# Performance work log

Hardware: AMD Instinct MI355X
Metric: run time of the kernel (lower is better)

The kernel has to match this reference:

```python
import jax, jax.numpy as jnp
import numpy as np

G, N, H = 64, 512, 64          # graphs, nodes/graph, hidden
NT = G * N                     # total nodes
DEG = 32
ET = NT * DEG                  # total edges
KP = int(np.ceil(0.7 * N))     # TopKPooling keep per graph (359)
NP2 = G * KP                   # nodes after pooling
F_IN, NC, NA = 128, 2, 6
seg = jax.ops.segment_sum


def graph_norm(h, batch, num_g, w, b, ms, eps=1e-5):
    cnt = seg(jnp.ones((h.shape[0], 1), h.dtype), batch, num_segments=num_g)
    mean = seg(h, batch, num_segments=num_g) / cnt
    hc = h - ms * mean[batch]
    var = seg(hc * hc, batch, num_segments=num_g) / cnt
    return w * hc / jnp.sqrt(var[batch] + eps) + b


def sage(h, src, tgt, valid, Ws, Wn, b, n_nodes):
    # PyG SAGEConv (mean aggr): out_i = x_i@Ws + mean_{j->i} x_j @ Wn + b
    msg = h[src] * valid[:, None]
    agg = seg(msg, tgt, num_segments=n_nodes)
    deg = seg(valid, tgt, num_segments=n_nodes)
    return h @ Ws + (agg / jnp.maximum(deg, 1.0)[:, None]) @ Wn + b


def setup_inputs() -> dict:
    key = jax.random.key(0)
    ks = jax.random.split(key, 20)
    offs = (jnp.arange(G) * N)[:, None]
    src = (jax.random.randint(ks[0], (G, N * DEG), 0, N) + offs).reshape(-1)
    tgt = (jax.random.randint(ks[1], (G, N * DEG), 0, N) + offs).reshape(-1)
    edge_index = jnp.stack([src, tgt])  # within-graph edges

    def lin(k, fi, fo):
        return jax.random.normal(k, (fi, fo), jnp.float32) / np.sqrt(fi)

    return {
        "x": jax.random.normal(ks[2], (NT, F_IN), jnp.float32),
        "edge_index": edge_index,
        "edge_attr": jax.random.uniform(ks[3], (ET,), jnp.float32),
        "coords": jax.random.normal(ks[4], (NT, 3), jnp.float32),
        "anatomical_class": jax.random.randint(ks[5], (NT,), 0, NA),
        "Bk_table": jax.random.normal(ks[6], (NA, H * H), jnp.float32) * 0.05,
        "pos_W": lin(ks[7], 3, H), "pos_b": jnp.zeros((H,), jnp.float32),
        "W1_self": lin(ks[8], F_IN, H), "W1_neigh": lin(ks[9], F_IN, H),
        "b1": jnp.zeros((H,), jnp.float32),
        "gn1_w": jnp.ones((H,), jnp.float32), "gn1_b": jnp.zeros((H,), jnp.float32),
        "gn1_ms": jnp.ones((H,), jnp.float32),
        "pool_p": jax.random.normal(ks[10], (H,), jnp.float32),
        "W2_self": lin(ks[11], H, H), "W2_neigh": lin(ks[12], H, H),
        "b2": jnp.zeros((H,), jnp.float32),
        "gn2_w": jnp.ones((H,), jnp.float32), "gn2_b": jnp.zeros((H,), jnp.float32),
        "gn2_ms": jnp.ones((H,), jnp.float32),
        "lin1_W": lin(ks[13], 3 * H, H), "lin1_b": jnp.zeros((H,), jnp.float32),
        "lin2_W": lin(ks[14], H, NC), "lin2_b": jnp.zeros((NC,), jnp.float32),
    }


def reference(x, edge_index, edge_attr, coords, anatomical_class, Bk_table,
              pos_W, pos_b, W1_self, W1_neigh, b1, gn1_w, gn1_b, gn1_ms,
              pool_p, W2_self, W2_neigh, b2, gn2_w, gn2_b, gn2_ms,
              lin1_W, lin1_b, lin2_W, lin2_b):
    row, col = edge_index[0], edge_index[1]
    batch = jnp.repeat(jnp.arange(G), N)
    # ---- stage 1: anatomical propagation kernel ----
    e = coords @ pos_W + pos_b                                 # [NT, H]
    Ae = seg(edge_attr[:, None] * e[col], row, num_segments=NT)  # SpMM adj @ e
    Bk = Bk_table[anatomical_class].reshape(NT, H, H)
    delta = jnp.einsum('nd,nhd->nh', Ae, Bk)                   # bmm(Ae, Bk^T)
    ones_e = jnp.ones((ET,), x.dtype)
    h = sage(x, row, col, ones_e, W1_self, W1_neigh, b1, NT)
    h = jax.nn.elu(graph_norm(h, batch, G, gn1_w, gn1_b, gn1_ms))
    h = h + delta
    h = jnp.einsum('nij,nj->ni', Bk + delta[:, :, None], h)    # propagate_message
    # ---- TopK pooling (equal-sized graphs) ----
    score = (h @ pool_p) / jnp.linalg.norm(pool_p)
    vals, idx = jax.lax.top_k(score.reshape(G, N), KP)
    perm = (idx + (jnp.arange(G) * N)[:, None]).reshape(-1)    # [NP2]
    h = h[perm] * jnp.tanh(vals).reshape(-1)[:, None]
    batch2 = jnp.repeat(jnp.arange(G), KP)
    node_map = jnp.full((NT,), -1, jnp.int32).at[perm].set(jnp.arange(NP2, dtype=jnp.int32))
    s2, t2 = node_map[row], node_map[col]
    valid = ((s2 >= 0) & (t2 >= 0)).astype(h.dtype)            # masked edge filter
    s2 = jnp.where(s2 >= 0, s2, 0)
    t2 = jnp.where(t2 >= 0, t2, 0)
    # ---- stage 2 ----
    e2 = coords[perm] @ pos_W + pos_b
    Bk2 = Bk_table[anatomical_class[perm]].reshape(NP2, H, H)
    Ae2 = seg(valid[:, None] * e2[t2], s2, num_segments=NP2)   # edge_attr = ones
    delta2 = jnp.einsum('nd,nhd->nh', Ae2, Bk2)
    h = h + delta2
    h = jnp.einsum('nij,nj->ni', Bk2 + delta2[:, :, None], h)
    h = sage(h, s2, t2, valid, W2_self, W2_neigh, b2, NP2)
    h = jax.nn.elu(graph_norm(h, batch2, G, gn2_w, gn2_b, gn2_ms))
    # ---- readout ----
    cnt = seg(jnp.ones((NP2, 1), h.dtype), batch2, num_segments=G)
    hsum = seg(h, batch2, num_segments=G)
    g = jnp.concatenate([hsum / cnt,
                         jax.ops.segment_max(h, batch2, num_segments=G),
                         hsum], axis=1)
    g = jax.nn.relu(g @ lin1_W + lin1_b)
    return jax.nn.log_softmax(g @ lin2_W + lin2_b, axis=1)
```

## Files before the change

### kernel.cpp

```cpp
#include <hip/hip_runtime.h>
#include <math.h>

#define G_    64
#define N_    512
#define H_    64
#define NT_   32768
#define ET_   1048576
#define EPG_  16384
#define KP_   359
#define NP2_  22976
#define FIN_  128
#define ESL_  2048
#define BPB_  (EPG_/ESL_)

__global__ __launch_bounds__(256)
void k_histprep(const int* __restrict__ row, const int* __restrict__ col,
                int* __restrict__ histR8, int* __restrict__ histC8,
                const float* __restrict__ Bk, const float* __restrict__ posW,
                const float* __restrict__ posb,
                float* __restrict__ BkT, float* __restrict__ PT) {
    int b = blockIdx.x, t = threadIdx.x;
    if (b < G_ * BPB_) {
        __shared__ int hr[N_], hc[N_];
        int g = b >> 3, s = b & (BPB_ - 1);
        for (int i = t; i < N_; i += 256) { hr[i] = 0; hc[i] = 0; }
        __syncthreads();
        int ebase = g * EPG_ + s * ESL_;
        for (int i = t; i < ESL_; i += 256) {
            atomicAdd(&hr[row[ebase + i] & (N_ - 1)], 1);
            atomicAdd(&hc[col[ebase + i] & (N_ - 1)], 1);
        }
        __syncthreads();
        int sbase = (g * BPB_ + s) * N_;
        for (int i = t; i < N_; i += 256) {
            histR8[sbase + i] = hr[i];
            histC8[sbase + i] = hc[i];
        }
    } else if (b < G_ * BPB_ + 96) {
        int idx = (b - G_ * BPB_) * 256 + t;
        int c = idx >> 12, r = idx & 4095;
        int h = r >> 6, d = r & 63;
        BkT[c * 4096 + d * 64 + h] = Bk[c * 4096 + h * 64 + d];
    } else {
        int c = b - (G_ * BPB_ + 96);
        int i = t >> 6, h = t & 63;
        const float* B = Bk + c * 4096 + h * 64;
        float acc = 0.f;
        for (int d = 0; d < 64; d++) {
            float vd = (i < 3) ? posW[i*64 + d] : posb[d];
            acc += B[d] * vd;
        }
        PT[c*256 + i*64 + h] = acc;
    }
}

__global__ __launch_bounds__(256)
void k_scan(const int* __restrict__ histR8, const int* __restrict__ histC8,
            int* __restrict__ rowptr, int* __restrict__ colptr,
            float* __restrict__ deg, int* __restrict__ nmap) {
    __shared__ int hr[N_], hc[N_];
    int g = blockIdx.x, t = threadIdx.x;
    int nbase = g * N_;
    for (int i = t; i < N_; i += 256) {
        int sr = 0, sc = 0;
        #pragma unroll
        for (int s = 0; s < BPB_; s++) {
            sr += histR8[(g * BPB_ + s) * N_ + i];
            sc += histC8[(g * BPB_ + s) * N_ + i];
        }
        hr[i] = sr; hc[i] = sc;
        deg[nbase + i] = (float)sc;
        nmap[nbase + i] = -1;
    }
    __syncthreads();
    int wave = t >> 6, lane = t & 63;
    if (wave < 2) {
        int* h = wave ? hc : hr;
        int base8 = lane * 8;
        int loc[8];
        int tot = 0;
        #pragma unroll
        for (int i = 0; i < 8; i++) { int v = h[base8 + i]; loc[i] = tot; tot += v; }
        int pref = tot;
        for (int off = 1; off < 64; off <<= 1) {
            int u = __shfl_up(pref, off);
            if (lane >= off) pref += u;
        }
        pref -= tot;
        #pragma unroll
        for (int i = 0; i < 8; i++) h[base8 + i] = pref + loc[i];
    }
    __syncthreads();
    int ebase = g * EPG_;
    for (int i = t; i < N_; i += 256) {
        rowptr[nbase + i] = ebase + hr[i];
        colptr[nbase + i] = ebase + hc[i];
    }
    if (g == 0 && t == 0) { rowptr[NT_] = ET_; colptr[NT_] = ET_; }
}

__global__ __launch_bounds__(1024)
void k_scat(const int* __restrict__ row, const int* __restrict__ col,
            const float* __restrict__ ea,
            const int* __restrict__ rowptr, const int* __restrict__ colptr,
            int2* __restrict__ rowcsr, int* __restrict__ colcsr) {
    __shared__ int curR[128], curC[128];
    int g = blockIdx.x >> 2, q = blockIdx.x & 3;
    int t = threadIdx.x;
    int lo = q * 128;
    int nbase = g * N_ + lo;
    if (t < 128) { curR[t] = rowptr[nbase + t]; curC[t] = colptr[nbase + t]; }
    __syncthreads();
    int ebase = g * EPG_;
    for (int i = t; i < EPG_; i += 1024) {
        int rg = row[ebase + i];
        int cg = col[ebase + i];
        int rl = (rg & (N_ - 1)) - lo;
        if ((unsigned)rl < 128u) {
            int pr = atomicAdd(&curR[rl], 1);
            rowcsr[pr] = make_int2(cg, __float_as_int(ea[ebase + i]));
        }
        int cl = (cg & (N_ - 1)) - lo;
        if ((unsigned)cl < 128u) {
            int pc = atomicAdd(&curC[cl], 1);
            colcsr[pc] = rg;
        }
    }
}

__global__ __launch_bounds__(256)
void k_gemm_dual(const float* __restrict__ in, int K,
                 const float* __restrict__ Wa, const float* __restrict__ Wb,
                 const float* __restrict__ bias,
                 float* __restrict__ outA, float* __restrict__ outB) {
    __shared__ float inT[32 * FIN_];
    int row0 = blockIdx.x * 32;
    int t = threadIdx.x;
    for (int idx = t; idx < 32 * K; idx += 256) inT[idx] = in[row0 * K + idx];
    __syncthreads();
    int c = t & 63, rb = t >> 6;
    const float* ip = inT + (rb * 8) * K;
    float aA[8] = {0,0,0,0,0,0,0,0};
    float aB[8] = {0,0,0,0,0,0,0,0};
    for (int k = 0; k < K; k += 4) {
        float wa0 = Wa[(k+0)*64 + c], wa1 = Wa[(k+1)*64 + c];
        float wa2 = Wa[(k+2)*64 + c], wa3 = Wa[(k+3)*64 + c];
        float wb0 = Wb[(k+0)*64 + c], wb1 = Wb[(k+1)*64 + c];
        float wb2 = Wb[(k+2)*64 + c], wb3 = Wb[(k+3)*64 + c];
        #pragma unroll
        for (int r = 0; r < 8; r++) {
            float4 xv = *(const float4*)&ip[r*K + k];
            aA[r] += xv.x*wa0; aB[r] += xv.x*wb0;
            aA[r] += xv.y*wa1; aB[r] += xv.y*wb1;
            aA[r] += xv.z*wa2; aB[r] += xv.z*wb2;
            aA[r] += xv.w*wa3; aB[r] += xv.w*wb3;
        }
    }
    float bv = bias[c];
    #pragma unroll
    for (int r = 0; r < 8; r++) {
        int node = row0 + rb*8 + r;
        outA[node*64 + c] = aA[r];
        outB[node*64 + c] = aB[r] + bv;
    }
}

__global__ __launch_bounds__(256)
void k_edge1f(const int* __restrict__ rowptr, const int2* __restrict__ rcsr,
              const int* __restrict__ colptr, const int* __restrict__ ccsr,
              const float* __restrict__ coords, const float* __restrict__ y,
              float4* __restrict__ nsum, float* __restrict__ agg) {
    int node = blockIdx.x * 4 + (threadIdx.x >> 6);
    int lane = threadIdx.x & 63;
    int rs = rowptr[node], re = rowptr[node + 1];
    float sx = 0.f, sy = 0.f, sz = 0.f, sw = 0.f;
    for (int k = rs + lane; k < re; k += 64) {
        int2 ent = rcsr[k];
        int c = ent.x;
        float w = __int_as_float(ent.y);
        sx += w * coords[c*3+0];
        sy += w * coords[c*3+1];
        sz += w * coords[c*3+2];
        sw += w;
    }
    #pragma unroll
    for (int off = 32; off; off >>= 1) {
        sx += __shfl_xor(sx, off); sy += __shfl_xor(sy, off);
        sz += __shfl_xor(sz, off); sw += __shfl_xor(sw, off);
    }
    if (lane == 0) nsum[node] = make_float4(sx, sy, sz, sw);
    int cs = colptr[node], ce = colptr[node + 1];
    float acc = 0.f;
    #pragma unroll 8
    for (int k = cs; k < ce; k++) {
        int r = ccsr[k];
        acc += y[r*64 + lane];
    }
    agg[node*64 + lane] = acc;
}

__global__ __launch_bounds__(256)
void k_gnstat(const float* __restrict__ hs, const float* __restrict__ agg,
              const float* __restrict__ deg, float* __restrict__ partial,
              int NPG, int CH, int npc) {
    __shared__ float r1[256], r2[256];
    int b = blockIdx.x;
    int g = b / CH, chunk = b % CH;
    int t = threadIdx.x, c = t & 63, grp = t >> 6;
    int n0 = chunk * npc;
    int nend = min(n0 + npc, NPG);
    float s1 = 0.f, s2 = 0.f;
    for (int n = n0 + grp; n < nend; n += 4) {
        int node = g * NPG + n;
        float v = hs[node*64 + c] + agg[node*64 + c] / fmaxf(deg[node], 1.f);
        s1 += v; s2 += v * v;
    }
    r1[t] = s1; r2[t] = s2;
    __syncthreads();
    if (grp == 0) {
        partial[b*128 + c]      = r1[c] + r1[64+c] + r1[128+c] + r1[192+c];
        partial[b*128 + 64 + c] = r2[c] + r2[64+c] + r2[128+c] + r2[192+c];
    }
}

__global__ __launch_bounds__(256)
void k_gnprop(const float* __restrict__ hself, const float* __restrict__ agg,
              const float* __restrict__ deg, const float* __restrict__ partial,
              const float* __restrict__ ms,
              const float* __restrict__ w, const float* __restrict__ b,
              const float4* __restrict__ nsum, const int* __restrict__ cls,
              const float* __restrict__ PT, const float* __restrict__ BkT,
              float* __restrict__ out) {
    __shared__ float hT[256];
    int t = threadIdx.x;
    int node = blockIdx.x * 4 + (t >> 6);
    int lane = t & 63;
    int g = (blockIdx.x * 4) >> 9;
    float s1 = 0.f, s2 = 0.f;
    #pragma unroll
    for (int i = 0; i < 8; i++) {
        s1 += partial[(g*8 + i)*128 + lane];
        s2 += partial[(g*8 + i)*128 + 64 + lane];
    }
    float m  = s1 / (float)N_, q = s2 / (float)N_, msv = ms[lane];
    float var = q - msv * m * m * (2.f - msv);
    float mval = msv * m;
    float istd = rsqrtf(var + 1e-5f);
    float4 s4 = nsum[node];
    int c = cls[node];
    const float* P = PT + c * 256;
    float d = s4.x*P[lane] + s4.y*P[64+lane] + s4.z*P[128+lane] + s4.w*P[192+lane];
    float v = hself[node*64 + lane] + agg[node*64 + lane] / fmaxf(deg[node], 1.f);
    v = w[lane] * (v - mval) * istd + b[lane];
    v = v > 0.f ? v : expm1f(v);
    v += d;
    hT[t] = v;
    __syncthreads();
    float ssum = v;
    #pragma unroll
    for (int off = 32; off; off >>= 1) ssum += __shfl_xor(ssum, off);
    const float* B  = BkT + c * 4096;
    const float* hv = hT + (t & ~63);
    float acc = 0.f;
    #pragma unroll 8
    for (int j = 0; j < 64; j++) acc += B[j*64 + lane] * hv[j];
    out[node*64 + lane] = acc + d * ssum;
}

__global__ __launch_bounds__(512)
void k_topk(const float* __restrict__ hp, const float* __restrict__ p,
            const int* __restrict__ cls, const int* __restrict__ ccsr,
            int* __restrict__ perm, float* __restrict__ tanhv,
            int* __restrict__ node_map, int* __restrict__ class2,
            int* __restrict__ ccsr2) {
    __shared__ float key[N_];
    __shared__ int   idxS[N_];
    __shared__ int   lmap[N_];
    __shared__ float pS[64];
    __shared__ float nrm;
    int g = blockIdx.x, t = threadIdx.x;
    lmap[t] = -1;
    if (t < 64) pS[t] = p[t];
    __syncthreads();
    if (t == 0) {
        float s = 0.f;
        for (int i = 0; i < 64; i++) s += pS[i] * pS[i];
        nrm = sqrtf(s);
    }
    __syncthreads();
    {
        float acc = 0.f;
        const float* hv = hp + (size_t)(g*N_ + t) * 64;
        for (int cdx = 0; cdx < 64; cdx++) acc += hv[cdx] * pS[cdx];
        key[t]  = acc / nrm;
        idxS[t] = t;
    }
    __syncthreads();
    for (int k = 2; k <= N_; k <<= 1) {
        for (int j = k >> 1; j > 0; j >>= 1) {
            int i = t, ixj = i ^ j;
            if (ixj > i) {
                float ki = key[i], kj = key[ixj];
                int   ii = idxS[i], ij = idxS[ixj];
                bool before = (ki > kj) || (ki == kj && ii < ij);
                bool dir = ((i & k) == 0);
                if (dir ? !before : before) {
                    key[i] = kj; key[ixj] = ki;
                    idxS[i] = ij; idxS[ixj] = ii;
                }
            }
            __syncthreads();
        }
    }
    if (t < KP_) {
        int orig  = idxS[t];
        int gnode = g * N_ + orig;
        int pj    = g * KP_ + t;
        perm[pj]     = gnode;
        tanhv[pj]    = tanhf(key[t]);
        node_map[gnode] = pj;
        class2[pj]   = cls[gnode];
        lmap[orig]   = pj;
    }
    __syncthreads();
    int ebase = g * EPG_;
    for (int k = t; k < EPG_; k += 512) {
        int mm = lmap[ccsr[ebase + k] & (N_ - 1)];
        ccsr2[ebase + k] = (mm >= 0) ? mm : NP2_;
    }
}

__global__ __launch_bounds__(256)
void k_s2prop(const int* __restrict__ rowptr, const int2* __restrict__ rcsr,
              const int* __restrict__ colptr, const int* __restrict__ ccsr,
              const int* __restrict__ perm, const int* __restrict__ nmap,
              const float* __restrict__ coords,
              const float* __restrict__ hp, const float* __restrict__ tanhv,
              const int* __restrict__ cls2,
              const float* __restrict__ PT, const float* __restrict__ BkT,
              float* __restrict__ out, float* __restrict__ deg2,
              float* __restrict__ y2zero) {
    __shared__ float hT[256];
    int t = threadIdx.x;
    int j = blockIdx.x * 4 + (t >> 6);
    int lane = t & 63;
    if (blockIdx.x == 0 && t < 64) y2zero[t] = 0.f;
    int orig = perm[j];
    int rs = rowptr[orig], re = rowptr[orig + 1];
    float sx = 0.f, sy = 0.f, sz = 0.f, sw = 0.f;
    for (int k = rs + lane; k < re; k += 64) {
        int c = rcsr[k].x;
        if (nmap[c] >= 0) {
            sx += coords[c*3+0]; sy += coords[c*3+1]; sz += coords[c*3+2];
            sw += 1.f;
        }
    }
    int cs = colptr[orig], ce = colptr[orig + 1];
    float dg = 0.f;
    for (int k = cs + lane; k < ce; k += 64) {
        if (nmap[ccsr[k]] >= 0) dg += 1.f;
    }
    #pragma unroll
    for (int off = 32; off; off >>= 1) {
        sx += __shfl_xor(sx, off); sy += __shfl_xor(sy, off);
        sz += __shfl_xor(sz, off); sw += __shfl_xor(sw, off);
        dg += __shfl_xor(dg, off);
    }
    if (lane == 0) deg2[j] = dg;
    int c = cls2[j];
    const float* P = PT + c * 256;
    float d = sx*P[lane] + sy*P[64+lane] + sz*P[128+lane] + sw*P[192+lane];
    float v = hp[orig*64 + lane] * tanhv[j] + d;
    hT[t] = v;
    __syncthreads();
    float ssum = v;
    #pragma unroll
    for (int off = 32; off; off >>= 1) ssum += __shfl_xor(ssum, off);
    const float* B  = BkT + c * 4096;
    const float* hv = hT + (t & ~63);
    float acc = 0.f;
    #pragma unroll 8
    for (int jj = 0; jj < 64; jj++) acc += B[jj*64 + lane] * hv[jj];
    out[j*64 + lane] = acc + d * ssum;
}

__global__ __launch_bounds__(256)
void k_gagg2(const int* __restrict__ colptr, const int* __restrict__ ccsr2,
             const int* __restrict__ perm, const float* __restrict__ y2,
             float* __restrict__ agg2) {
    int j = blockIdx.x * 4 + (threadIdx.x >> 6);
    int lane = threadIdx.x & 63;
    int orig = perm[j];
    int start = colptr[orig], end = colptr[orig + 1];
    float acc = 0.f;
    #pragma unroll 8
    for (int k = start; k < end; k++) {
        int r = ccsr2[k];
        acc += y2[r*64 + lane];
    }
    agg2[j*64 + lane] = acc;
}

__global__ __launch_bounds__(256)
void k_gnrd(const float* __restrict__ hs, const float* __restrict__ agg,
            const float* __restrict__ deg2, const float* __restrict__ statsP,
            const float* __restrict__ ms,
            const float* __restrict__ w, const float* __restrict__ b,
            float* __restrict__ readP) {
    __shared__ float r1[256], r2[256];
    int blk = blockIdx.x;
    int g = blk / 6, chunk = blk % 6;
    int t = threadIdx.x, c = t & 63, grp = t >> 6;
    float s1 = 0.f, s2 = 0.f;
    #pragma unroll
    for (int i = 0; i < 6; i++) {
        s1 += statsP[(g*6 + i)*128 + c];
        s2 += statsP[(g*6 + i)*128 + 64 + c];
    }
    float mean = s1 / (float)KP_, q = s2 / (float)KP_, msv = ms[c];
    float var = q - msv * mean * mean * (2.f - msv);
    float mv = msv * mean;
    float is = rsqrtf(var + 1e-5f);
    float wv = w[c], bv = b[c];
    int n0 = chunk * 60, nend = min(n0 + 60, KP_);
    float s = 0.f, m = -1e30f;
    for (int n = n0 + grp; n < nend; n += 4) {
        int node = g * KP_ + n;
        float v = hs[node*64 + c] + agg[node*64 + c] / fmaxf(deg2[node], 1.f);
        v = wv * (v - mv) * is + bv;
        v = v > 0.f ? v : expm1f(v);
        s += v; m = fmaxf(m, v);
    }
    r1[t] = s; r2[t] = m;
    __syncthreads();
    if (grp == 0) {
        readP[blk*128 + c]      = r1[c] + r1[64+c] + r1[128+c] + r1[192+c];
        readP[blk*128 + 64 + c] = fmaxf(fmaxf(r2[c], r2[64+c]), fmaxf(r2[128+c], r2[192+c]));
    }
}

__global__ void k_rfin(const float* __restrict__ part, int CH,
                       const float* __restrict__ l1W, const float* __restrict__ l1b,
                       const float* __restrict__ l2W, const float* __restrict__ l2b,
                       float* __restrict__ out) {
    __shared__ float gv[192], rS[64];
    int g = blockIdx.x, t = threadIdx.x;
    float s = 0.f, m = -1e30f;
    for (int i = 0; i < CH; i++) {
        s += part[(g*CH + i)*128 + t];
        m = fmaxf(m, part[(g*CH + i)*128 + 64 + t]);
    }
    gv[t] = s / (float)KP_;
    gv[64 + t] = m;
    gv[128 + t] = s;
    __syncthreads();
    float acc = l1b[t];
    for (int k = 0; k < 192; k++) acc += gv[k] * l1W[k*64 + t];
    rS[t] = fmaxf(acc, 0.f);
    __syncthreads();
    if (t == 0) {
        float l0 = l2b[0], l1v = l2b[1];
        for (int hh = 0; hh < 64; hh++) { l0 += rS[hh]*l2W[hh*2+0]; l1v += rS[hh]*l2W[hh*2+1]; }
        float mx  = fmaxf(l0, l1v);
        float lse = mx + logf(expf(l0 - mx) + expf(l1v - mx));
        out[g*2 + 0] = l0  - lse;
        out[g*2 + 1] = l1v - lse;
    }
}

extern "C" void kernel_launch(void* const* d_in, const int* in_sizes, int n_in,
                              void* d_out, int out_size, void* d_ws, size_t ws_size,
                              hipStream_t stream) {
    const float* x      = (const float*)d_in[0];
    const int*   eidx   = (const int*)  d_in[1];
    const float* eattr  = (const float*)d_in[2];
    const float* coords = (const float*)d_in[3];
    const int*   acls   = (const int*)  d_in[4];
    const float* BkTab  = (const float*)d_in[5];
    const float* posW   = (const float*)d_in[6];
    const float* posb   = (const float*)d_in[7];
    const float* W1s    = (const float*)d_in[8];
    const float* W1n    = (const float*)d_in[9];
    const float* b1     = (const float*)d_in[10];
    const float* gn1w   = (const float*)d_in[11];
    const float* gn1b   = (const float*)d_in[12];
    const float* gn1ms  = (const float*)d_in[13];
    const float* poolp  = (const float*)d_in[14];
    const float* W2s    = (const float*)d_in[15];
    const float* W2n    = (const float*)d_in[16];
    const float* b2     = (const float*)d_in[17];
    const float* gn2w   = (const float*)d_in[18];
    const float* gn2b   = (const float*)d_in[19];
    const float* gn2ms  = (const float*)d_in[20];
    const float* l1W    = (const float*)d_in[21];
    const float* l1b    = (const float*)d_in[22];
    const float* l2W    = (const float*)d_in[23];
    const float* l2b    = (const float*)d_in[24];

    const int* row  = eidx;
    const int* colp = eidx + ET_;

    float* W = (float*)d_ws;
    const size_t NTH = (size_t)NT_ * 64;
    float* b0    = W;
    float* b1buf = W + 1*NTH;
    float* b2buf = W + 2*NTH;
    float* b3buf = W + 3*NTH;
    float* p = W + 4*NTH;
    int2*  rowcsr = (int2*)p;        p += 2*(size_t)ET_;
    int*   colcsr = (int*)p;         p += ET_;
    int*   ccsr2  = (int*)p;         p += ET_;
    int*   rowptr = (int*)p;         p += NT_ + 8;
    int*   colptr = (int*)p;         p += NT_ + 8;
    int*   histR8 = (int*)p;         p += NT_ * BPB_ / 1;
    int*   histC8 = (int*)p;         p += NT_ * BPB_ / 1;
    float* deg    = p;               p += NT_;
    float* deg2   = p;               p += NP2_;
    float* tanhv  = p;               p += NP2_;
    int*   perm   = (int*)p;         p += NP2_;
    int*   nmap   = (int*)p;         p += NT_;
    int*   cls2   = (int*)p;         p += NP2_;
    float* BkT    = p;               p += 6 * 4096;
    float* PT     = p;               p += 6 * 256;
    float* statsP = p;               p += (size_t)G_ * 8 * 128;
    float* readP  = p;               p += (size_t)G_ * 6 * 128;
    float4* nsum  = (float4*)b3buf;

    k_histprep <<<G_*BPB_ + 102, 256, 0, stream>>>(row, colp, histR8, histC8,
                                                   BkTab, posW, posb, BkT, PT);
    k_scan     <<<G_,      256,  0, stream>>>(histR8, histC8, rowptr, colptr, deg, nmap);
    k_scat     <<<G_*4,    1024, 0, stream>>>(row, colp, eattr, rowptr, colptr,
                                              rowcsr, colcsr);

    k_gemm_dual<<<NT_/32,  256, 0, stream>>>(x, FIN_, W1n, W1s, b1,
                                             b0 , b1buf );
    k_edge1f   <<<NT_/4,   256, 0, stream>>>(rowptr, rowcsr, colptr, colcsr,
                                             coords, b0 , nsum, b2buf );
    k_gnstat   <<<G_*8,    256, 0, stream>>>(b1buf , b2buf , deg,
                                             statsP, N_, 8, 64);
    k_gnprop   <<<NT_/4,   256, 0, stream>>>(b1buf , b2buf , deg,
                                             statsP, gn1ms, gn1w, gn1b,
                                             nsum, acls, PT, BkT,
                                             b1buf );
    k_topk     <<<G_,      512, 0, stream>>>(b1buf , poolp, acls, colcsr,
                                             perm, tanhv, nmap, cls2, ccsr2);

    k_s2prop   <<<NP2_/4,  256, 0, stream>>>(rowptr, rowcsr, colptr, colcsr,
                                             perm, nmap, coords,
                                             b1buf , tanhv, cls2, PT, BkT,
                                             b2buf , deg2,
                                             b0 + (size_t)NP2_ * 64 );
    k_gemm_dual<<<NP2_/32, 256, 0, stream>>>(b2buf , 64, W2n, W2s, b2,
                                             b0 , b3buf );
    k_gagg2    <<<NP2_/4,  256, 0, stream>>>(colptr, ccsr2, perm, b0 ,
                                             b1buf );
    k_gnstat   <<<G_*6,    256, 0, stream>>>(b3buf , b1buf , deg2,
                                             statsP, KP_, 6, 60);
    k_gnrd     <<<G_*6,    256, 0, stream>>>(b3buf , b1buf , deg2,
                                             statsP, gn2ms, gn2w, gn2b, readP);
    k_rfin     <<<G_,      64,  0, stream>>>(readP, 6, l1W, l1b, l2W, l2b,
                                             (float*)d_out);
}
```

Baseline: 335.2 us.

## Fuse scan, CSR scatter, stage-1 edge aggregation and GN stats into one kernel

Merges the per-graph prefix scan, CSR scatter, stage-1 neighbor aggregation and graph-norm statistics into a single 1024-thread kernel. Each block handles a quarter of a graph and reads back the CSR it just wrote. This removes three launches and the intermediate round-trips of rowptr/colptr and the aggregation buffer. Stage-2 degree counting moves from a colcsr walk in k_s2prop to a shared-memory histogram in k_topk. The cost is much lower parallelism for the aggregation phase (256 blocks instead of 8192 waves' worth), which risks latency-bound gathers.

```diff
diff --git a/kernel.cpp b/kernel.cpp
--- a/kernel.cpp
+++ b/kernel.cpp
@@ -3,15 +3,12 @@
 
 #define G_    64
 #define N_    512
-#define H_    64
 #define NT_   32768
 #define ET_   1048576
 #define EPG_  16384
 #define KP_   359
 #define NP2_  22976
 #define FIN_  128
-#define ESL_  2048
-#define BPB_  (EPG_/ESL_)
 
 __global__ __launch_bounds__(256)
 void k_histprep(const int* __restrict__ row, const int* __restrict__ col,
@@ -20,111 +17,37 @@
                 const float* __restrict__ posb,
                 float* __restrict__ BkT, float* __restrict__ PT) {
     int b = blockIdx.x, t = threadIdx.x;
-    if (b < G_ * BPB_) {
+    if (b < 512) {
         __shared__ int hr[N_], hc[N_];
-        int g = b >> 3, s = b & (BPB_ - 1);
+        int g = b >> 3, s = b & 7;
         for (int i = t; i < N_; i += 256) { hr[i] = 0; hc[i] = 0; }
         __syncthreads();
-        int ebase = g * EPG_ + s * ESL_;
-        for (int i = t; i < ESL_; i += 256) {
+        int ebase = g * EPG_ + s * 2048;
+        for (int i = t; i < 2048; i += 256) {
             atomicAdd(&hr[row[ebase + i] & (N_ - 1)], 1);
             atomicAdd(&hc[col[ebase + i] & (N_ - 1)], 1);
         }
         __syncthreads();
-        int sbase = (g * BPB_ + s) * N_;
+        int sbase = b * N_;
         for (int i = t; i < N_; i += 256) {
             histR8[sbase + i] = hr[i];
             histC8[sbase + i] = hc[i];
         }
-    } else if (b < G_ * BPB_ + 96) {
-        int idx = (b - G_ * BPB_) * 256 + t;
+    } else if (b < 608) {
+        int idx = (b - 512) * 256 + t;
         int c = idx >> 12, r = idx & 4095;
         int h = r >> 6, d = r & 63;
-        BkT[c * 4096 + d * 64 + h] = Bk[c * 4096 + h * 64 + d];
+        BkT[c*4096 + d*64 + h] = Bk[c*4096 + h*64 + d];
     } else {
-        int c = b - (G_ * BPB_ + 96);
+        int c = b - 608;
         int i = t >> 6, h = t & 63;
-        const float* B = Bk + c * 4096 + h * 64;
+        const float* B = Bk + c*4096 + h*64;
         float acc = 0.f;
         for (int d = 0; d < 64; d++) {
             float vd = (i < 3) ? posW[i*64 + d] : posb[d];
             acc += B[d] * vd;
         }
         PT[c*256 + i*64 + h] = acc;
-    }
-}
-
-__global__ __launch_bounds__(256)
-void k_scan(const int* __restrict__ histR8, const int* __restrict__ histC8,
-            int* __restrict__ rowptr, int* __restrict__ colptr,
-            float* __restrict__ deg, int* __restrict__ nmap) {
-    __shared__ int hr[N_], hc[N_];
-    int g = blockIdx.x, t = threadIdx.x;
-    int nbase = g * N_;
-    for (int i = t; i < N_; i += 256) {
-        int sr = 0, sc = 0;
-        #pragma unroll
-        for (int s = 0; s < BPB_; s++) {
-            sr += histR8[(g * BPB_ + s) * N_ + i];
-            sc += histC8[(g * BPB_ + s) * N_ + i];
-        }
-        hr[i] = sr; hc[i] = sc;
-        deg[nbase + i] = (float)sc;
-        nmap[nbase + i] = -1;
-    }
-    __syncthreads();
-    int wave = t >> 6, lane = t & 63;
-    if (wave < 2) {
-        int* h = wave ? hc : hr;
-        int base8 = lane * 8;
-        int loc[8];
-        int tot = 0;
-        #pragma unroll
-        for (int i = 0; i < 8; i++) { int v = h[base8 + i]; loc[i] = tot; tot += v; }
-        int pref = tot;
-        for (int off = 1; off < 64; off <<= 1) {
-            int u = __shfl_up(pref, off);
-            if (lane >= off) pref += u;
-        }
-        pref -= tot;
-        #pragma unroll
-        for (int i = 0; i < 8; i++) h[base8 + i] = pref + loc[i];
-    }
-    __syncthreads();
-    int ebase = g * EPG_;
-    for (int i = t; i < N_; i += 256) {
-        rowptr[nbase + i] = ebase + hr[i];
-        colptr[nbase + i] = ebase + hc[i];
-    }
-    if (g == 0 && t == 0) { rowptr[NT_] = ET_; colptr[NT_] = ET_; }
-}
-
-__global__ __launch_bounds__(1024)
-void k_scat(const int* __restrict__ row, const int* __restrict__ col,
-            const float* __restrict__ ea,
-            const int* __restrict__ rowptr, const int* __restrict__ colptr,
-            int2* __restrict__ rowcsr, int* __restrict__ colcsr) {
-    __shared__ int curR[128], curC[128];
-    int g = blockIdx.x >> 2, q = blockIdx.x & 3;
-    int t = threadIdx.x;
-    int lo = q * 128;
-    int nbase = g * N_ + lo;
-    if (t < 128) { curR[t] = rowptr[nbase + t]; curC[t] = colptr[nbase + t]; }
-    __syncthreads();
-    int ebase = g * EPG_;
-    for (int i = t; i < EPG_; i += 1024) {
-        int rg = row[ebase + i];
-        int cg = col[ebase + i];
-        int rl = (rg & (N_ - 1)) - lo;
-        if ((unsigned)rl < 128u) {
-            int pr = atomicAdd(&curR[rl], 1);
-            rowcsr[pr] = make_int2(cg, __float_as_int(ea[ebase + i]));
-        }
-        int cl = (cg & (N_ - 1)) - lo;
-        if ((unsigned)cl < 128u) {
-            int pc = atomicAdd(&curC[cl], 1);
-            colcsr[pc] = rg;
-        }
     }
 }
 
@@ -165,38 +88,129 @@
     }
 }
 
-__global__ __launch_bounds__(256)
-void k_edge1f(const int* __restrict__ rowptr, const int2* __restrict__ rcsr,
-              const int* __restrict__ colptr, const int* __restrict__ ccsr,
-              const float* __restrict__ coords, const float* __restrict__ y,
-              float4* __restrict__ nsum, float* __restrict__ agg) {
-    int node = blockIdx.x * 4 + (threadIdx.x >> 6);
-    int lane = threadIdx.x & 63;
-    int rs = rowptr[node], re = rowptr[node + 1];
-    float sx = 0.f, sy = 0.f, sz = 0.f, sw = 0.f;
-    for (int k = rs + lane; k < re; k += 64) {
-        int2 ent = rcsr[k];
-        int c = ent.x;
-        float w = __int_as_float(ent.y);
-        sx += w * coords[c*3+0];
-        sy += w * coords[c*3+1];
-        sz += w * coords[c*3+2];
-        sw += w;
-    }
-    #pragma unroll
-    for (int off = 32; off; off >>= 1) {
-        sx += __shfl_xor(sx, off); sy += __shfl_xor(sy, off);
-        sz += __shfl_xor(sz, off); sw += __shfl_xor(sw, off);
-    }
-    if (lane == 0) nsum[node] = make_float4(sx, sy, sz, sw);
-    int cs = colptr[node], ce = colptr[node + 1];
-    float acc = 0.f;
-    #pragma unroll 8
-    for (int k = cs; k < ce; k++) {
-        int r = ccsr[k];
-        acc += y[r*64 + lane];
-    }
-    agg[node*64 + lane] = acc;
+__global__ __launch_bounds__(1024)
+void k_scatfuse(const int* __restrict__ row, const int* __restrict__ col,
+                const float* __restrict__ ea,
+                const int* __restrict__ histR8, const int* __restrict__ histC8,
+                const float* __restrict__ coords, const float* __restrict__ y,
+                const float* __restrict__ hself,
+                int2* __restrict__ rowcsr, int* __restrict__ colcsr,
+                int* __restrict__ rowptr, int* __restrict__ colptr,
+                float* __restrict__ deg, int* __restrict__ nmap,
+                float4* __restrict__ nsum, float* __restrict__ agg,
+                float* __restrict__ statsP) {
+    __shared__ int hr[N_], hc[N_];
+    __shared__ int rst[128], rcn[128], cst[128], ccn[128];
+    __shared__ float red[2048];
+    int g = blockIdx.x >> 2, q = blockIdx.x & 3;
+    int t = threadIdx.x;
+    int lo = q * 128;
+    int nbase = g * N_, ebase = g * EPG_;
+    for (int i = t; i < N_; i += 1024) {
+        int sr = 0, sc = 0;
+        #pragma unroll
+        for (int s = 0; s < 8; s++) {
+            sr += histR8[(g*8 + s)*N_ + i];
+            sc += histC8[(g*8 + s)*N_ + i];
+        }
+        hr[i] = sr; hc[i] = sc;
+    }
+    __syncthreads();
+    int wave = t >> 6, lane = t & 63;
+    if (wave < 2) {
+        int* h = wave ? hc : hr;
+        int base8 = lane * 8;
+        int loc[8];
+        int tot = 0;
+        #pragma unroll
+        for (int i = 0; i < 8; i++) { int v = h[base8 + i]; loc[i] = tot; tot += v; }
+        int pref = tot;
+        for (int off = 1; off < 64; off <<= 1) {
+            int u = __shfl_up(pref, off);
+            if (lane >= off) pref += u;
+        }
+        pref -= tot;
+        #pragma unroll
+        for (int i = 0; i < 8; i++) h[base8 + i] = pref + loc[i];
+    }
+    __syncthreads();
+    if (t < 128) {
+        int i = lo + t;
+        int rs = hr[i];
+        int re = (i < N_ - 1) ? hr[i + 1] : EPG_;
+        int cs = hc[i];
+        int ce = (i < N_ - 1) ? hc[i + 1] : EPG_;
+        rst[t] = ebase + rs; rcn[t] = re - rs;
+        cst[t] = ebase + cs; ccn[t] = ce - cs;
+        rowptr[nbase + i] = ebase + rs;
+        colptr[nbase + i] = ebase + cs;
+        deg[nbase + i] = (float)(ce - cs);
+        nmap[nbase + i] = -1;
+    }
+    if (blockIdx.x == 0 && t == 0) { rowptr[NT_] = ET_; colptr[NT_] = ET_; }
+    __syncthreads();
+    for (int i = t; i < EPG_; i += 1024) {
+        int rg = row[ebase + i];
+        int cg = col[ebase + i];
+        int rl = (rg & (N_ - 1)) - lo;
+        if ((unsigned)rl < 128u) {
+            int pr = atomicAdd(&hr[lo + rl], 1);
+            rowcsr[ebase + pr] = make_int2(cg, __float_as_int(ea[ebase + i]));
+        }
+        int cl = (cg & (N_ - 1)) - lo;
+        if ((unsigned)cl < 128u) {
+            int pc = atomicAdd(&hc[lo + cl], 1);
+            colcsr[ebase + pc] = rg;
+        }
+    }
+    __threadfence_block();
+    __syncthreads();
+    float s1 = 0.f, s2 = 0.f;
+    #pragma unroll
+    for (int r = 0; r < 8; r++) {
+        int li   = wave * 8 + r;
+        int node = nbase + lo + li;
+        int rs = rst[li], rc = rcn[li];
+        float sx = 0.f, sy = 0.f, sz = 0.f, sw = 0.f;
+        for (int k = lane; k < rc; k += 64) {
+            int2 ent = rowcsr[rs + k];
+            int c = ent.x;
+            float w = __int_as_float(ent.y);
+            sx += w * coords[c*3+0];
+            sy += w * coords[c*3+1];
+            sz += w * coords[c*3+2];
+            sw += w;
+        }
+        #pragma unroll
+        for (int off = 32; off; off >>= 1) {
+            sx += __shfl_xor(sx, off); sy += __shfl_xor(sy, off);
+            sz += __shfl_xor(sz, off); sw += __shfl_xor(sw, off);
+        }
+        if (lane == 0) nsum[node] = make_float4(sx, sy, sz, sw);
+        int cs = cst[li], cc = ccn[li];
+        float acc = 0.f;
+        #pragma unroll 8
+        for (int k = 0; k < cc; k++) {
+            int rr = colcsr[cs + k];
+            acc += y[rr*64 + lane];
+        }
+        agg[node*64 + lane] = acc;
+        float v = hself[node*64 + lane] + acc / fmaxf((float)cc, 1.f);
+        s1 += v; s2 += v * v;
+    }
+    red[wave*64 + lane]        = s1;
+    red[1024 + wave*64 + lane] = s2;
+    __syncthreads();
+    if (t < 64) {
+        float a1 = 0.f, a2 = 0.f;
+        #pragma unroll
+        for (int wv = 0; wv < 16; wv++) {
+            a1 += red[wv*64 + t];
+            a2 += red[1024 + wv*64 + t];
+        }
+        statsP[blockIdx.x*128 + t]      = a1;
+        statsP[blockIdx.x*128 + 64 + t] = a2;
+    }
 }
 
 __global__ __launch_bounds__(256)
@@ -238,9 +252,9 @@
     int g = (blockIdx.x * 4) >> 9;
     float s1 = 0.f, s2 = 0.f;
     #pragma unroll
-    for (int i = 0; i < 8; i++) {
-        s1 += partial[(g*8 + i)*128 + lane];
-        s2 += partial[(g*8 + i)*128 + 64 + lane];
+    for (int i = 0; i < 4; i++) {
+        s1 += partial[(g*4 + i)*128 + lane];
+        s2 += partial[(g*4 + i)*128 + 64 + lane];
     }
     float m  = s1 / (float)N_, q = s2 / (float)N_, msv = ms[lane];
     float var = q - msv * m * m * (2.f - msv);
@@ -270,17 +284,20 @@
 __global__ __launch_bounds__(512)
 void k_topk(const float* __restrict__ hp, const float* __restrict__ p,
             const int* __restrict__ cls, const int* __restrict__ ccsr,
+            const int* __restrict__ row, const int* __restrict__ col,
             int* __restrict__ perm, float* __restrict__ tanhv,
             int* __restrict__ node_map, int* __restrict__ class2,
-            int* __restrict__ ccsr2) {
+            int* __restrict__ ccsr2, float* __restrict__ deg2) {
     __shared__ float key[N_];
     __shared__ int   idxS[N_];
     __shared__ int   lmap[N_];
+    __shared__ int   ideg[KP_];
     __shared__ float pS[64];
     __shared__ float nrm;
     int g = blockIdx.x, t = threadIdx.x;
     lmap[t] = -1;
     if (t < 64) pS[t] = p[t];
+    for (int i = t; i < KP_; i += 512) ideg[i] = 0;
     __syncthreads();
     if (t == 0) {
         float s = 0.f;
@@ -328,18 +345,23 @@
         int mm = lmap[ccsr[ebase + k] & (N_ - 1)];
         ccsr2[ebase + k] = (mm >= 0) ? mm : NP2_;
     }
+    for (int k = t; k < EPG_; k += 512) {
+        int mr = lmap[row[ebase + k] & (N_ - 1)];
+        int mc = lmap[col[ebase + k] & (N_ - 1)];
+        if (mr >= 0 && mc >= 0) atomicAdd(&ideg[mc - g * KP_], 1);
+    }
+    __syncthreads();
+    for (int i = t; i < KP_; i += 512) deg2[g * KP_ + i] = (float)ideg[i];
 }
 
 __global__ __launch_bounds__(256)
 void k_s2prop(const int* __restrict__ rowptr, const int2* __restrict__ rcsr,
-              const int* __restrict__ colptr, const int* __restrict__ ccsr,
               const int* __restrict__ perm, const int* __restrict__ nmap,
               const float* __restrict__ coords,
               const float* __restrict__ hp, const float* __restrict__ tanhv,
               const int* __restrict__ cls2,
               const float* __restrict__ PT, const float* __restrict__ BkT,
-              float* __restrict__ out, float* __restrict__ deg2,
-              float* __restrict__ y2zero) {
+              float* __restrict__ out, float* __restrict__ y2zero) {
     __shared__ float hT[256];
     int t = threadIdx.x;
     int j = blockIdx.x * 4 + (t >> 6);
@@ -355,18 +377,11 @@
             sw += 1.f;
         }
     }
-    int cs = colptr[orig], ce = colptr[orig + 1];
-    float dg = 0.f;
-    for (int k = cs + lane; k < ce; k += 64) {
-        if (nmap[ccsr[k]] >= 0) dg += 1.f;
-    }
     #pragma unroll
     for (int off = 32; off; off >>= 1) {
         sx += __shfl_xor(sx, off); sy += __shfl_xor(sy, off);
         sz += __shfl_xor(sz, off); sw += __shfl_xor(sw, off);
-        dg += __shfl_xor(dg, off);
-    }
-    if (lane == 0) deg2[j] = dg;
+    }
     int c = cls2[j];
     const float* P = PT + c * 256;
     float d = sx*P[lane] + sy*P[64+lane] + sz*P[128+lane] + sw*P[192+lane];
@@ -512,8 +527,8 @@
     int*   ccsr2  = (int*)p;         p += ET_;
     int*   rowptr = (int*)p;         p += NT_ + 8;
     int*   colptr = (int*)p;         p += NT_ + 8;
-    int*   histR8 = (int*)p;         p += NT_ * BPB_ / 1;
-    int*   histC8 = (int*)p;         p += NT_ * BPB_ / 1;
+    int*   histR8 = (int*)p;         p += NT_ * 8;
+    int*   histC8 = (int*)p;         p += NT_ * 8;
     float* deg    = p;               p += NT_;
     float* deg2   = p;               p += NP2_;
     float* tanhv  = p;               p += NP2_;
@@ -526,29 +541,26 @@
     float* readP  = p;               p += (size_t)G_ * 6 * 128;
     float4* nsum  = (float4*)b3buf;
 
-    k_histprep <<<G_*BPB_ + 102, 256, 0, stream>>>(row, colp, histR8, histC8,
-                                                   BkTab, posW, posb, BkT, PT);
-    k_scan     <<<G_,      256,  0, stream>>>(histR8, histC8, rowptr, colptr, deg, nmap);
-    k_scat     <<<G_*4,    1024, 0, stream>>>(row, colp, eattr, rowptr, colptr,
-                                              rowcsr, colcsr);
-
+    k_histprep <<<614,     256,  0, stream>>>(row, colp, histR8, histC8,
+                                              BkTab, posW, posb, BkT, PT);
     k_gemm_dual<<<NT_/32,  256, 0, stream>>>(x, FIN_, W1n, W1s, b1,
                                              b0 , b1buf );
-    k_edge1f   <<<NT_/4,   256, 0, stream>>>(rowptr, rowcsr, colptr, colcsr,
-                                             coords, b0 , nsum, b2buf );
-    k_gnstat   <<<G_*8,    256, 0, stream>>>(b1buf , b2buf , deg,
-                                             statsP, N_, 8, 64);
+    k_scatfuse <<<G_*4,    1024, 0, stream>>>(row, colp, eattr, histR8, histC8,
+                                              coords, b0 , b1buf ,
+                                              rowcsr, colcsr, rowptr, colptr,
+                                              deg, nmap, nsum, b2buf ,
+                                              statsP);
     k_gnprop   <<<NT_/4,   256, 0, stream>>>(b1buf , b2buf , deg,
                                              statsP, gn1ms, gn1w, gn1b,
                                              nsum, acls, PT, BkT,
                                              b1buf );
     k_topk     <<<G_,      512, 0, stream>>>(b1buf , poolp, acls, colcsr,
-                                             perm, tanhv, nmap, cls2, ccsr2);
-
-    k_s2prop   <<<NP2_/4,  256, 0, stream>>>(rowptr, rowcsr, colptr, colcsr,
-                                             perm, nmap, coords,
+                                             row, colp, perm, tanhv, nmap,
+                                             cls2, ccsr2, deg2);
+
+    k_s2prop   <<<NP2_/4,  256, 0, stream>>>(rowptr, rowcsr, perm, nmap, coords,
                                              b1buf , tanhv, cls2, PT, BkT,
-                                             b2buf , deg2,
+                                             b2buf ,
                                              b0 + (size_t)NP2_ * 64 );
     k_gemm_dual<<<NP2_/32, 256, 0, stream>>>(b2buf , 64, W2n, W2s, b2,
                                              b0 , b3buf );
```

Result: no change. 341.7 us (+1.9%).
